# Kernel tuning notes

Hardware: AMD Instinct MI355X
Metric: run time of the kernel (lower is better)

The kernel has to match this reference:

```python
import jax, jax.numpy as jnp
import numpy as np

B = 256
D = 2048          # in_channels (shared latent dim)
S = 8             # n_subjects
OUT = 1000        # sum of 7 Schaefer network head widths [150,148,132,136,76,122,236]


def setup_inputs() -> dict:
    key = jax.random.key(0)
    k1, k2, k3, k4 = jax.random.split(key, 4)
    x = jax.random.normal(k1, (B, D), dtype=jnp.float32)
    subject_ids = jax.random.randint(k2, (B,), 0, S, dtype=jnp.int64)
    scale = 1.0 / np.sqrt(D)  # matches normal_(0, 1/in_channels**0.5)
    # Concatenated per-head weights: equivalent to 7 heads of shapes
    # (S, D, n_k) concatenated along the output axis (n_k sums to OUT).
    W = jax.random.normal(k3, (S, D, OUT), dtype=jnp.float32) * scale
    b = jax.random.normal(k4, (S, OUT), dtype=jnp.float32) * scale
    return {"x": x, "subject_ids": subject_ids, "W": W, "b": b}


def reference(x, subject_ids, W, b):
    # Per-sample weight gather (B, D, OUT) followed by batched matmul,
    # exactly mirroring torch: w = weights[subject_ids]; einsum('bd,bdo->bo').
    w = W[subject_ids]                      # (B, D, OUT) gathered copy
    out = jnp.einsum('bd,bdo->bo', x, w)    # (B, OUT)
    out = out + b[subject_ids]              # per-subject bias
    return out
```

## Files before the change

kernel.cpp:

```cpp
#include <hip/hip_runtime.h>
#include <stdint.h>

#define Bn   256
#define Dn   2048
#define Sn   8
#define ON   1000

#define ROWS 64
#define OT   256
#define KS   256
#define NDC  (Dn / KS)
#define STK  32
#define NST  (KS / STK)
#define LDKS 40
#define BUFB (OT * LDKS * 2)

typedef short v8s __attribute__((ext_vector_type(8)));
typedef short v4s __attribute__((ext_vector_type(4)));
typedef float v4f __attribute__((ext_vector_type(4)));

static __device__ __forceinline__ short f2bf(float f) {
    union { float f; uint32_t u; } v; v.f = f;
    uint32_t u = v.u;
    u += 0x7FFFu + ((u >> 16) & 1u);
    return (short)(u >> 16);
}

__global__ __launch_bounds__(256) void gather_kernel(const float* __restrict__ x,
                                                     const int* __restrict__ sid,
                                                     unsigned short* __restrict__ xg) {
    __shared__ unsigned long long bmask[4];
    __shared__ int brow;
    const int r = blockIdx.x;
    const int s = blockIdx.y;
    const int t = threadIdx.x;
    const int lane = t & 63;
    const int wave = t >> 6;

    const bool match = (sid[t] == s);
    const unsigned long long m = __ballot(match);
    if (lane == 0) bmask[wave] = m;
    if (t == 0) brow = -1;
    __syncthreads();
    if (match) {
        int pos = __popcll(m & ((1ull << lane) - 1ull));
        for (int w = 0; w < wave; ++w) pos += __popcll(bmask[w]);
        if (pos == r) brow = t;
    }
    __syncthreads();

    const int b = brow;
    v8s v = (v8s){0, 0, 0, 0, 0, 0, 0, 0};
    if (b >= 0) {
        const float4 f0 = *(const float4*)(x + (size_t)b * Dn + t * 8);
        const float4 f1 = *(const float4*)(x + (size_t)b * Dn + t * 8 + 4);
        v[0] = f2bf(f0.x); v[1] = f2bf(f0.y); v[2] = f2bf(f0.z); v[3] = f2bf(f0.w);
        v[4] = f2bf(f1.x); v[5] = f2bf(f1.y); v[6] = f2bf(f1.z); v[7] = f2bf(f1.w);
    }
    *(v8s*)(xg + ((size_t)s * ROWS + r) * Dn + t * 8) = v;
}

__global__ __launch_bounds__(512) void main_kernel(const unsigned short* __restrict__ xg,
                                                   const int* __restrict__ sid,
                                                   const float* __restrict__ W,
                                                   float* __restrict__ part) {
    __shared__ unsigned short Bsh[2][OT * LDKS];
    __shared__ unsigned long long bmask[8];
    __shared__ int rows_l[ROWS];

    const int oc = blockIdx.x;
    const int kc = blockIdx.y;
    const int s  = blockIdx.z;
    const int o0 = oc * OT;
    const int k0 = kc * KS;
    const int t  = threadIdx.x;
    const int lane = t & 63;
    const int w    = t >> 6;

    const int mysid = (t < Bn) ? sid[t] : -1;
    const bool match = (mysid == s);
    const unsigned long long m = __ballot(match);
    if (lane == 0) bmask[w] = m;
    if (t < ROWS) rows_l[t] = -1;
    __syncthreads();
    if (match) {
        int pos = __popcll(m & ((1ull << lane) - 1ull));
        for (int ww = 0; ww < w; ++ww) pos += __popcll(bmask[ww]);
        if (pos < ROWS) rows_l[pos] = t;
    }
    __syncthreads();

    int og = o0 + 4 * lane;
    if (og > ON - 4) og = ON - 4;
    const float* wpb = W + ((size_t)s * Dn + k0 + 4 * w) * ON + og;

    unsigned short* wr[4];
#pragma unroll
    for (int i = 0; i < 4; ++i)
        wr[i] = (unsigned short*)((char*)&Bsh[0][0]
                + (4 * lane + i) * 80 + 16 * ((w >> 1) ^ (lane & 3)) + 8 * (w & 1));

    const int lo16 = lane & 15;
    const int quad = lane >> 4;
    const int arow = (w >> 1) * 16 + lo16;
    const bool wactive = (rows_l[(w >> 1) * 16] >= 0);
    const unsigned short* xr = xg + ((size_t)s * ROWS + arow) * Dn + k0 + quad * 8;

    v8s af[NST];
#pragma unroll
    for (int st = 0; st < NST; ++st) af[st] = *(const v8s*)(xr + st * STK);

    const int rb0  = (w & 1) * 128 + lo16;
    const int rswz = 16 * (quad ^ ((lo16 >> 2) & 3));

    v4f fb[2][4];
#pragma unroll
    for (int c = 0; c < 2; ++c)
#pragma unroll
        for (int r = 0; r < 4; ++r)
            fb[c][r] = *(const v4f*)(wpb + ((size_t)c * STK + r) * ON);

    v4f acc[8];
#pragma unroll
    for (int i = 0; i < 8; ++i) acc[i] = (v4f){0.f, 0.f, 0.f, 0.f};

#pragma unroll
    for (int st = 0; st < NST; ++st) {
        const int sl = st & 1;
#pragma unroll
        for (int i = 0; i < 4; ++i) {
            v4s kv;
            kv[0] = f2bf(fb[sl][0][i]);
            kv[1] = f2bf(fb[sl][1][i]);
            kv[2] = f2bf(fb[sl][2][i]);
            kv[3] = f2bf(fb[sl][3][i]);
            *(v4s*)((char*)wr[i] + sl * BUFB) = kv;
        }
        if (st + 2 < NST) {
#pragma unroll
            for (int r = 0; r < 4; ++r)
                fb[sl][r] = *(const v4f*)(wpb + ((size_t)(st + 2) * STK + r) * ON);
        }
        asm volatile("s_waitcnt lgkmcnt(0)" ::: "memory");
        __builtin_amdgcn_s_barrier();
        asm volatile("" ::: "memory");

        if (wactive) {
            const v8s a = af[st];
            const char* bb = (const char*)&Bsh[sl][0];
#pragma unroll
            for (int nt = 0; nt < 8; ++nt) {
                const v8s bf = *(const v8s*)(bb + (rb0 + nt * 16) * 80 + rswz);
                acc[nt] = __builtin_amdgcn_mfma_f32_16x16x32_bf16(a, bf, acc[nt],
                                                                  0, 0, 0);
            }
        }
    }

    if (wactive) {
        float* pp = part + (size_t)kc * Bn * ON;
        const int er0 = (w >> 1) * 16 + quad * 4;
#pragma unroll
        for (int nt = 0; nt < 8; ++nt) {
            const int o = o0 + (w & 1) * 128 + nt * 16 + lo16;
            if (o < ON) {
#pragma unroll
                for (int r = 0; r < 4; ++r) {
                    const int bi = rows_l[er0 + r];
                    if (bi >= 0) pp[(size_t)bi * ON + o] = acc[nt][r];
                }
            }
        }
    }
}

__global__ __launch_bounds__(256) void reduce_kernel(const int* __restrict__ sid,
                                                     const float* __restrict__ bias,
                                                     const float* __restrict__ part,
                                                     float* __restrict__ out) {
    const int b = blockIdx.x;
    const int s = sid[b];
    const int o = threadIdx.x * 4;
    if (o < ON) {
        float4 v = *(const float4*)(bias + (size_t)s * ON + o);
#pragma unroll
        for (int d = 0; d < NDC; d++) {
            const float4 p = *(const float4*)(part + ((size_t)d * Bn + b) * ON + o);
            v.x += p.x; v.y += p.y; v.z += p.z; v.w += p.w;
        }
        *(float4*)(out + (size_t)b * ON + o) = v;
    }
}

extern "C" void kernel_launch(void* const* d_in, const int* in_sizes, int n_in,
                              void* d_out, int out_size, void* d_ws, size_t ws_size,
                              hipStream_t stream) {
    const float* x    = (const float*)d_in[0];
    const int*   sid  = (const int*)d_in[1];
    const float* W    = (const float*)d_in[2];
    const float* bias = (const float*)d_in[3];
    float*       out  = (float*)d_out;
    float*       part = (float*)d_ws;
    unsigned short* xg = (unsigned short*)((char*)d_ws + (size_t)NDC * Bn * ON * sizeof(float));

    gather_kernel<<<dim3(ROWS, Sn), dim3(256), 0, stream>>>(x, sid, xg);
    main_kernel<<<dim3(4, NDC, Sn), dim3(512), 0, stream>>>(xg, sid, W, part);
    reduce_kernel<<<dim3(Bn), dim3(256), 0, stream>>>(sid, bias, part, out);
}
```

Before: 108.7 us.

## Fuse x gather and bf16 conversion into main GEMM kernel, deepen W prefetch

Removes the separate gather kernel and has the main kernel read fp32 rows of x directly via the per-subject row list, converting them to bf16 in registers. This drops one kernel launch and the bf16 staging buffer round-trip. The global W register prefetch also grows from two stages to three, so loads are issued further ahead at the cost of more VGPRs, which may lower occupancy. x rows are now re-read in fp32 by each output-tile block, so x traffic is higher.

```diff
diff --git a/kernel.cpp b/kernel.cpp
--- a/kernel.cpp
+++ b/kernel.cpp
@@ -26,41 +26,7 @@
     return (short)(u >> 16);
 }
 
-__global__ __launch_bounds__(256) void gather_kernel(const float* __restrict__ x,
-                                                     const int* __restrict__ sid,
-                                                     unsigned short* __restrict__ xg) {
-    __shared__ unsigned long long bmask[4];
-    __shared__ int brow;
-    const int r = blockIdx.x;
-    const int s = blockIdx.y;
-    const int t = threadIdx.x;
-    const int lane = t & 63;
-    const int wave = t >> 6;
-
-    const bool match = (sid[t] == s);
-    const unsigned long long m = __ballot(match);
-    if (lane == 0) bmask[wave] = m;
-    if (t == 0) brow = -1;
-    __syncthreads();
-    if (match) {
-        int pos = __popcll(m & ((1ull << lane) - 1ull));
-        for (int w = 0; w < wave; ++w) pos += __popcll(bmask[w]);
-        if (pos == r) brow = t;
-    }
-    __syncthreads();
-
-    const int b = brow;
-    v8s v = (v8s){0, 0, 0, 0, 0, 0, 0, 0};
-    if (b >= 0) {
-        const float4 f0 = *(const float4*)(x + (size_t)b * Dn + t * 8);
-        const float4 f1 = *(const float4*)(x + (size_t)b * Dn + t * 8 + 4);
-        v[0] = f2bf(f0.x); v[1] = f2bf(f0.y); v[2] = f2bf(f0.z); v[3] = f2bf(f0.w);
-        v[4] = f2bf(f1.x); v[5] = f2bf(f1.y); v[6] = f2bf(f1.z); v[7] = f2bf(f1.w);
-    }
-    *(v8s*)(xg + ((size_t)s * ROWS + r) * Dn + t * 8) = v;
-}
-
-__global__ __launch_bounds__(512) void main_kernel(const unsigned short* __restrict__ xg,
+__global__ __launch_bounds__(512) void main_kernel(const float* __restrict__ x,
                                                    const int* __restrict__ sid,
                                                    const float* __restrict__ W,
                                                    float* __restrict__ part) {
@@ -103,22 +69,37 @@
     const int lo16 = lane & 15;
     const int quad = lane >> 4;
     const int arow = (w >> 1) * 16 + lo16;
+    const int xrow = rows_l[arow];
     const bool wactive = (rows_l[(w >> 1) * 16] >= 0);
-    const unsigned short* xr = xg + ((size_t)s * ROWS + arow) * Dn + k0 + quad * 8;
+    const float* xp = (xrow >= 0 ? x + (size_t)xrow * Dn : x) + k0 + quad * 8;
+
+    float4 a0[NST], a1[NST];
+#pragma unroll
+    for (int st = 0; st < NST; ++st) {
+        a0[st] = *(const float4*)(xp + st * STK);
+        a1[st] = *(const float4*)(xp + st * STK + 4);
+    }
+
+    v4f fb[3][4];
+#pragma unroll
+    for (int c = 0; c < 3; ++c)
+#pragma unroll
+        for (int r = 0; r < 4; ++r)
+            fb[c][r] = *(const v4f*)(wpb + ((size_t)c * STK + r) * ON);
 
     v8s af[NST];
 #pragma unroll
-    for (int st = 0; st < NST; ++st) af[st] = *(const v8s*)(xr + st * STK);
+    for (int st = 0; st < NST; ++st) {
+        v8s a;
+        a[0] = f2bf(a0[st].x); a[1] = f2bf(a0[st].y);
+        a[2] = f2bf(a0[st].z); a[3] = f2bf(a0[st].w);
+        a[4] = f2bf(a1[st].x); a[5] = f2bf(a1[st].y);
+        a[6] = f2bf(a1[st].z); a[7] = f2bf(a1[st].w);
+        af[st] = a;
+    }
 
     const int rb0  = (w & 1) * 128 + lo16;
     const int rswz = 16 * (quad ^ ((lo16 >> 2) & 3));
-
-    v4f fb[2][4];
-#pragma unroll
-    for (int c = 0; c < 2; ++c)
-#pragma unroll
-        for (int r = 0; r < 4; ++r)
-            fb[c][r] = *(const v4f*)(wpb + ((size_t)c * STK + r) * ON);
 
     v4f acc[8];
 #pragma unroll
@@ -127,19 +108,20 @@
 #pragma unroll
     for (int st = 0; st < NST; ++st) {
         const int sl = st & 1;
+        const int rg = st % 3;
 #pragma unroll
         for (int i = 0; i < 4; ++i) {
             v4s kv;
-            kv[0] = f2bf(fb[sl][0][i]);
-            kv[1] = f2bf(fb[sl][1][i]);
-            kv[2] = f2bf(fb[sl][2][i]);
-            kv[3] = f2bf(fb[sl][3][i]);
+            kv[0] = f2bf(fb[rg][0][i]);
+            kv[1] = f2bf(fb[rg][1][i]);
+            kv[2] = f2bf(fb[rg][2][i]);
+            kv[3] = f2bf(fb[rg][3][i]);
             *(v4s*)((char*)wr[i] + sl * BUFB) = kv;
         }
-        if (st + 2 < NST) {
+        if (st + 3 < NST) {
 #pragma unroll
             for (int r = 0; r < 4; ++r)
-                fb[sl][r] = *(const v4f*)(wpb + ((size_t)(st + 2) * STK + r) * ON);
+                fb[rg][r] = *(const v4f*)(wpb + ((size_t)(st + 3) * STK + r) * ON);
         }
         asm volatile("s_waitcnt lgkmcnt(0)" ::: "memory");
         __builtin_amdgcn_s_barrier();
@@ -201,9 +183,7 @@
     const float* bias = (const float*)d_in[3];
     float*       out  = (float*)d_out;
     float*       part = (float*)d_ws;
-    unsigned short* xg = (unsigned short*)((char*)d_ws + (size_t)NDC * Bn * ON * sizeof(float));
 
-    gather_kernel<<<dim3(ROWS, Sn), dim3(256), 0, stream>>>(x, sid, xg);
-    main_kernel<<<dim3(4, NDC, Sn), dim3(512), 0, stream>>>(xg, sid, W, part);
+    main_kernel<<<dim3(4, NDC, Sn), dim3(512), 0, stream>>>(x, sid, W, part);
     reduce_kernel<<<dim3(Bn), dim3(256), 0, stream>>>(sid, bias, part, out);
 }
```

Result: no change. 107.3 us (median of 2 runs) (-1.3%).
